# Performance work log

Measured on AMD Instinct MI355X. Metric: run time of the kernel, lower is better.

The kernel has to match this reference:

```python
import jax, jax.numpy as jnp
import numpy as np

B, L = 4, 2048
D_MODEL, D_STATE, D_CONV, EXPAND = 1024, 16, 4, 2
D_INNER = EXPAND * D_MODEL
DT_RANK = D_MODEL // 16  # mamba-ssm default dt_rank = ceil(d_model/16)


def _mamba(x, in_w, conv_w, conv_b, xproj_w, dt_w, dt_b, A_log, D, out_w):
    # x: [B, L, d_model]; faithful port of mamba_ssm.Mamba forward (slow path math)
    di, ds = A_log.shape
    dt_rank = dt_w.shape[1]
    dc = conv_w.shape[1]
    xz = x @ in_w.T                          # [B, L, 2*di]
    xi, z = jnp.split(xz, 2, axis=-1)
    # causal depthwise conv over time
    xc = jnp.swapaxes(xi, 1, 2)              # [B, di, L]
    xc = jax.lax.conv_general_dilated(
        xc, conv_w[:, None, :], (1,), [(dc - 1, 0)],
        feature_group_count=di, dimension_numbers=('NCH', 'OIH', 'NCH'))
    xc = xc + conv_b[None, :, None]
    xi = jax.nn.silu(jnp.swapaxes(xc, 1, 2))  # [B, L, di]
    proj = xi @ xproj_w.T                    # [B, L, dt_rank + 2*ds]
    dt, Bm, Cm = jnp.split(proj, [dt_rank, dt_rank + ds], axis=-1)
    delta = jax.nn.softplus(dt @ dt_w.T + dt_b)  # [B, L, di]
    A = -jnp.exp(A_log)                      # [di, ds]

    def step(h, t):
        d_t, B_t, C_t, x_t = t               # [B,di],[B,ds],[B,ds],[B,di]
        h = jnp.exp(d_t[:, :, None] * A) * h + (d_t * x_t)[:, :, None] * B_t[:, None, :]
        return h, jnp.einsum('bds,bs->bd', h, C_t)

    xs = (jnp.swapaxes(delta, 0, 1), jnp.swapaxes(Bm, 0, 1),
          jnp.swapaxes(Cm, 0, 1), jnp.swapaxes(xi, 0, 1))
    h0 = jnp.zeros((x.shape[0], di, ds), x.dtype)
    _, ys = jax.lax.scan(step, h0, xs)       # ys: [L, B, di]
    y = jnp.swapaxes(ys, 0, 1) + xi * D
    y = y * jax.nn.silu(z)
    return y @ out_w.T


def setup_inputs() -> dict:
    ks = jax.random.split(jax.random.key(0), 24)

    def p(i, shape, scale=0.02):
        return jax.random.normal(ks[i], shape, jnp.float32) * scale

    inp = {
        'x': jax.random.normal(ks[0], (B, L, D_MODEL), jnp.float32),
        'ln_g': jnp.ones((D_MODEL,), jnp.float32),
        'ln_b': jnp.zeros((D_MODEL,), jnp.float32),
        'merge_w': p(1, (D_MODEL, 2 * D_MODEL)),
        'merge_b': jnp.zeros((D_MODEL,), jnp.float32),
    }
    for j, pre in enumerate(('fwd', 'bwd')):
        o = 2 + j * 8
        inp[pre + '_in_w'] = p(o, (2 * D_INNER, D_MODEL))
        inp[pre + '_conv_w'] = p(o + 1, (D_INNER, D_CONV), 0.3)
        inp[pre + '_conv_b'] = jnp.zeros((D_INNER,), jnp.float32)
        inp[pre + '_xproj_w'] = p(o + 2, (DT_RANK + 2 * D_STATE, D_INNER))
        inp[pre + '_dt_w'] = p(o + 3, (D_INNER, DT_RANK), 0.1)
        inp[pre + '_dt_b'] = -4.0 + p(o + 4, (D_INNER,), 0.5)
        inp[pre + '_A_log'] = jnp.broadcast_to(
            jnp.log(jnp.arange(1, D_STATE + 1, dtype=jnp.float32)), (D_INNER, D_STATE)) + 0.0
        inp[pre + '_D'] = jnp.ones((D_INNER,), jnp.float32)
        inp[pre + '_out_w'] = p(o + 5, (D_MODEL, D_INNER))
    return inp


def reference(x, ln_g, ln_b, merge_w, merge_b,
              fwd_in_w, fwd_conv_w, fwd_conv_b, fwd_xproj_w, fwd_dt_w, fwd_dt_b,
              fwd_A_log, fwd_D, fwd_out_w,
              bwd_in_w, bwd_conv_w, bwd_conv_b, bwd_xproj_w, bwd_dt_w, bwd_dt_b,
              bwd_A_log, bwd_D, bwd_out_w):
    mu = jnp.mean(x, axis=-1, keepdims=True)
    var = jnp.mean(jnp.square(x - mu), axis=-1, keepdims=True)
    xn = (x - mu) / jnp.sqrt(var + 1e-5) * ln_g + ln_b
    y_f = _mamba(xn, fwd_in_w, fwd_conv_w, fwd_conv_b, fwd_xproj_w, fwd_dt_w,
                 fwd_dt_b, fwd_A_log, fwd_D, fwd_out_w)
    y_b = jnp.flip(_mamba(jnp.flip(xn, 1), bwd_in_w, bwd_conv_w, bwd_conv_b,
                          bwd_xproj_w, bwd_dt_w, bwd_dt_b, bwd_A_log, bwd_D,
                          bwd_out_w), 1)
    y = jnp.concatenate([y_f, y_b], axis=-1) @ merge_w.T + merge_b
    return x + y
```

## Files before the change

kernel.cpp:

```cpp
#include <hip/hip_runtime.h>

typedef unsigned short u16;
typedef unsigned int u32;
typedef __attribute__((ext_vector_type(8))) short short8;
typedef __attribute__((ext_vector_type(8))) u16 ushort8v;
typedef __attribute__((ext_vector_type(4))) float float4v;
typedef __attribute__((ext_vector_type(4))) u16 ushort4v;

#define SEQ_L 2048
#define NTOK 8192
#define DMODEL 1024
#define DINNER 2048
#define NCH 32
#define CHL 64

__device__ __forceinline__ float bf2f(u16 v) { return __uint_as_float(((u32)v) << 16); }
__device__ __forceinline__ u16 f2bf(float f) {
    u32 u = __float_as_uint(f);
    return (u16)((u + 0x7FFFu + ((u >> 16) & 1u)) >> 16);
}
__device__ __forceinline__ float loadf(const void* p, size_t i, bool bf) {
    return bf ? bf2f(((const u16*)p)[i]) : ((const float*)p)[i];
}
__device__ __forceinline__ void gl2lds(const void* g, void* l) {
    __builtin_amdgcn_global_load_lds(
        (const __attribute__((address_space(1))) void*)g,
        (__attribute__((address_space(3))) void*)l, 16, 0, 0);
}

__global__ void detect_kernel(const u32* __restrict__ lng, int* __restrict__ flag) {
    if (threadIdx.x == 0) flag[0] = (lng[0] == 0x3F800000u) ? 0 : 1;
}

__global__ void cvt_kernel(const void* __restrict__ in, u16* __restrict__ out,
                           int n4, const int* __restrict__ flag) {
    int i = blockIdx.x * 256 + threadIdx.x;
    if (i >= n4) return;
    bool bf = flag[0] != 0;
    ushort4v o;
    if (bf) {
        o = ((const ushort4v*)in)[i];
    } else {
        float4v v = ((const float4v*)in)[i];
        o.x = f2bf(v.x); o.y = f2bf(v.y); o.z = f2bf(v.z); o.w = f2bf(v.w);
    }
    ((ushort4v*)out)[i] = o;
}

__global__ __launch_bounds__(256) void transpose_ow(const void* __restrict__ ow,
        u16* __restrict__ ot, const int* __restrict__ flag) {
    bool bf = flag[0] != 0;
    __shared__ u16 tile[32][33];
    int k0 = blockIdx.x * 32;
    int j0 = blockIdx.y * 32;
    int tx = threadIdx.x & 31;
    int ty = threadIdx.x >> 5;
    #pragma unroll
    for (int r = 0; r < 4; ++r) {
        int j = ty + r * 8;
        tile[j][tx] = f2bf(loadf(ow, (size_t)(j0 + j) * 2048 + k0 + tx, bf));
    }
    __syncthreads();
    #pragma unroll
    for (int r = 0; r < 4; ++r) {
        int k = ty + r * 8;
        ot[(size_t)(k0 + k) * 1024 + j0 + tx] = tile[tx][k];
    }
}

__global__ __launch_bounds__(256) void ln_kernel(const void* __restrict__ xin,
        const void* __restrict__ g, const void* __restrict__ be,
        u16* __restrict__ xn, const int* __restrict__ flag) {
    bool bf = flag[0] != 0;
    int tok = blockIdx.x;
    int tid = threadIdx.x;
    float v[4];
    if (bf) {
        ushort4v u = ((const ushort4v*)xin)[(size_t)tok * 256 + tid];
        v[0] = bf2f(u.x); v[1] = bf2f(u.y); v[2] = bf2f(u.z); v[3] = bf2f(u.w);
    } else {
        float4v f = ((const float4v*)xin)[(size_t)tok * 256 + tid];
        v[0] = f.x; v[1] = f.y; v[2] = f.z; v[3] = f.w;
    }
    float s = v[0] + v[1] + v[2] + v[3];
    float s2 = v[0]*v[0] + v[1]*v[1] + v[2]*v[2] + v[3]*v[3];
    for (int o = 1; o < 64; o <<= 1) { s += __shfl_xor(s, o); s2 += __shfl_xor(s2, o); }
    __shared__ float red[8];
    int w = tid >> 6;
    if ((tid & 63) == 0) { red[w] = s; red[4 + w] = s2; }
    __syncthreads();
    s = red[0] + red[1] + red[2] + red[3];
    s2 = red[4] + red[5] + red[6] + red[7];
    float mu = s * (1.f / 1024.f);
    float var = s2 * (1.f / 1024.f) - mu * mu;
    float rstd = rsqrtf(var + 1e-5f);
    int base = tid * 4;
    ushort4v o;
    o.x = f2bf((v[0] - mu) * rstd * loadf(g, base + 0, bf) + loadf(be, base + 0, bf));
    o.y = f2bf((v[1] - mu) * rstd * loadf(g, base + 1, bf) + loadf(be, base + 1, bf));
    o.z = f2bf((v[2] - mu) * rstd * loadf(g, base + 2, bf) + loadf(be, base + 2, bf));
    o.w = f2bf((v[3] - mu) * rstd * loadf(g, base + 3, bf) + loadf(be, base + 3, bf));
    ((ushort4v*)xn)[(size_t)tok * 256 + tid] = o;
}

__global__ __launch_bounds__(256) void build_wf(
    const void* __restrict__ dtw, const void* __restrict__ xpw,
    u16* __restrict__ wf, const int* __restrict__ flag)
{
    bool bf = flag[0] != 0;
    int n = blockIdx.x;
    int k0 = threadIdx.x * 8;
    ushort8v o;
    if (n >= DINNER) {
        int r = (n - DINNER) + 64;
        if (bf) {
            o = *(const ushort8v*)((const u16*)xpw + (size_t)r * 2048 + k0);
        } else {
            const float* p = (const float*)xpw + (size_t)r * 2048 + k0;
            #pragma unroll
            for (int j = 0; j < 8; ++j) o[j] = f2bf(p[j]);
        }
    } else {
        float acc[8];
        #pragma unroll
        for (int j = 0; j < 8; ++j) acc[j] = 0.f;
        for (int r = 0; r < 64; ++r) {
            float dw = loadf(dtw, (size_t)n * 64 + r, bf);
            if (bf) {
                ushort8v v = *(const ushort8v*)((const u16*)xpw + (size_t)r * 2048 + k0);
                #pragma unroll
                for (int j = 0; j < 8; ++j) acc[j] = fmaf(dw, bf2f(v[j]), acc[j]);
            } else {
                const float* p = (const float*)xpw + (size_t)r * 2048 + k0;
                #pragma unroll
                for (int j = 0; j < 8; ++j) acc[j] = fmaf(dw, p[j], acc[j]);
            }
        }
        #pragma unroll
        for (int j = 0; j < 8; ++j) o[j] = f2bf(acc[j]);
    }
    *(ushort8v*)(wf + (size_t)n * 2048 + k0) = o;
}

template<int EPI, bool FLIPA>
__global__ __launch_bounds__(256) void gemm_bt(
    const u16* __restrict__ A, int lda,
    const u16* __restrict__ W, int ldw,
    void* __restrict__ Cv, int ldc,
    int M, int N, int K,
    const void* __restrict__ bias, const void* __restrict__ resid,
    const int* __restrict__ flag)
{
    __shared__ u16 As[128 * 32];
    __shared__ u16 Ws[128 * 32];
    bool bf = flag[0] != 0;
    int tid = threadIdx.x;
    int lane = tid & 63;
    int wave = tid >> 6;
    int wm = wave >> 1, wn = wave & 1;
    int m0 = blockIdx.x * 128;
    int n0 = blockIdx.y * 128;
    int l15 = lane & 15;
    int quad = lane >> 4;

    int c0 = tid, c1 = tid + 256;
    int row0 = c0 >> 2, row1 = c1 >> 2;
    int kk0 = ((c0 & 3) ^ ((row0 ^ (row0 >> 1)) & 3)) << 3;
    int kk1 = ((c1 & 3) ^ ((row1 ^ (row1 >> 1)) & 3)) << 3;
    int ar0 = m0 + row0, ar1 = m0 + row1;
    if (FLIPA) {
        int b0 = ar0 >> 11, t0 = ar0 & (SEQ_L - 1); ar0 = (b0 << 11) | (SEQ_L - 1 - t0);
        int b1 = ar1 >> 11, t1 = ar1 & (SEQ_L - 1); ar1 = (b1 << 11) | (SEQ_L - 1 - t1);
    }
    int wr0 = n0 + row0; if (wr0 > N - 1) wr0 = N - 1;
    int wr1 = n0 + row1; if (wr1 > N - 1) wr1 = N - 1;
    const u16* Ag0 = A + (size_t)ar0 * lda + kk0;
    const u16* Ag1 = A + (size_t)ar1 * lda + kk1;
    const u16* Wg0 = W + (size_t)wr0 * ldw + kk0;
    const u16* Wg1 = W + (size_t)wr1 * ldw + kk1;
    u16* lA0 = &As[c0 * 8]; u16* lA1 = &As[c1 * 8];
    u16* lW0 = &Ws[c0 * 8]; u16* lW1 = &Ws[c1 * 8];

    int aoff[4], boff[4];
    #pragma unroll
    for (int i = 0; i < 4; ++i) {
        int ra = wm * 64 + i * 16 + l15;
        aoff[i] = ra * 32 + ((quad ^ ((ra ^ (ra >> 1)) & 3)) << 3);
        int rb = wn * 64 + i * 16 + l15;
        boff[i] = rb * 32 + ((quad ^ ((rb ^ (rb >> 1)) & 3)) << 3);
    }

    float4v acc[4][4] = {};

    for (int k0 = 0; k0 < K; k0 += 32) {
        __syncthreads();
        gl2lds(Ag0 + k0, lA0);
        gl2lds(Ag1 + k0, lA1);
        gl2lds(Wg0 + k0, lW0);
        gl2lds(Wg1 + k0, lW1);
        __syncthreads();
        short8 af[4], bfr[4];
        #pragma unroll
        for (int i = 0; i < 4; ++i) af[i] = *(const short8*)&As[aoff[i]];
        #pragma unroll
        for (int j = 0; j < 4; ++j) bfr[j] = *(const short8*)&Ws[boff[j]];
        #pragma unroll
        for (int i = 0; i < 4; ++i)
            #pragma unroll
            for (int j = 0; j < 4; ++j)
                acc[i][j] = __builtin_amdgcn_mfma_f32_16x16x32_bf16(af[i], bfr[j], acc[i][j], 0, 0, 0);
    }

    #pragma unroll
    for (int i = 0; i < 4; ++i) {
        #pragma unroll
        for (int j = 0; j < 4; ++j) {
            #pragma unroll
            for (int r = 0; r < 4; ++r) {
                int row = m0 + wm * 64 + i * 16 + quad * 4 + r;
                int col = n0 + wn * 64 + j * 16 + l15;
                if (col < N) {
                    float v = acc[i][j][r];
                    if (EPI == 0) {
                        ((u16*)Cv)[(size_t)row * ldc + col] = f2bf(v);
                    } else if (EPI == 2) {
                        v += loadf(bias, col, bf) + loadf(resid, (size_t)row * DMODEL + col, bf);
                        if (bf) ((u16*)Cv)[(size_t)row * ldc + col] = f2bf(v);
                        else    ((float*)Cv)[(size_t)row * ldc + col] = v;
                    } else if (EPI == 3) {
                        if (col < DINNER) {
                            v += loadf(bias, col, bf);
                            v = fmaxf(v, 0.f) + __logf(1.f + __expf(-fabsf(v)));
                            ((u16*)Cv)[(size_t)row * 4096 + col] = f2bf(v);
                        } else {
                            ((u16*)resid)[(size_t)row * 32 + (col - DINNER)] = f2bf(v);
                        }
                    } else {
                        if (bf) {
                            u16* p = (u16*)Cv + (size_t)row * ldc + col;
                            *p = f2bf(bf2f(*p) + v);
                        } else {
                            float* p = (float*)Cv + (size_t)row * ldc + col;
                            *p = *p + v;
                        }
                    }
                }
            }
        }
    }
}

__global__ __launch_bounds__(256) void conv_kernel(const u16* __restrict__ xz,
        const void* __restrict__ cw, const void* __restrict__ cb,
        u16* __restrict__ xc, const int* __restrict__ flag)
{
    bool bf = flag[0] != 0;
    int idx = blockIdx.x * 256 + threadIdx.x;
    int d = idx & (DINNER - 1);
    int t = (idx >> 11) & (SEQ_L - 1);
    int b = idx >> 22;
    float acc = loadf(cb, d, bf);
    #pragma unroll
    for (int k = 0; k < 4; ++k) {
        int tt = t - 3 + k;
        if (tt >= 0)
            acc += loadf(cw, d * 4 + k, bf) * bf2f(xz[((size_t)(b * SEQ_L + tt) << 12) + d]);
    }
    float r = acc / (1.f + __expf(-acc));
    xc[idx] = f2bf(r);
}


__global__ __launch_bounds__(256) void scan_pass1(
    const u16* __restrict__ xz, const u16* __restrict__ xc,
    const u16* __restrict__ proj, const void* __restrict__ A_log,
    float2* __restrict__ chk, const int* __restrict__ flag)
{
    bool bf = flag[0] != 0;
    int g = blockIdx.x * 256 + threadIdx.x;
    int d = g & (DINNER - 1);
    int c = (g >> 11) & (NCH - 1);
    int b = g >> 16;
    float Ac[16];
    #pragma unroll
    for (int s = 0; s < 16; ++s) Ac[s] = -__expf(loadf(A_log, (size_t)d * 16 + s, bf));
    size_t tok0 = (size_t)b * SEQ_L + c * CHL;
    const u16* dp = xz + tok0 * 4096 + d;
    const u16* xp = xc + tok0 * DINNER + d;
    const u16* bp = proj + tok0 * 32;
    float h[16];
    #pragma unroll
    for (int s = 0; s < 16; ++s) h[s] = 0.f;
    float sd = 0.f;
    for (int t = 0; t < CHL; ++t) {
        float dl = bf2f(*dp);
        float xi = bf2f(*xp);
        ushort8v bv0 = *(const ushort8v*)bp;
        ushort8v bv1 = *(const ushort8v*)(bp + 8);
        float u = dl * xi;
        #pragma unroll
        for (int s = 0; s < 16; ++s) {
            float a = __expf(dl * Ac[s]);
            float Bs = bf2f(s < 8 ? bv0[s] : bv1[s - 8]);
            h[s] = fmaf(a, h[s], u * Bs);
        }
        sd += dl;
        dp += 4096; xp += DINNER; bp += 32;
    }
    size_t base = (size_t)c * 131072 + ((size_t)b << 15) + d;
    #pragma unroll
    for (int s = 0; s < 16; ++s)
        chk[base + (size_t)s * 2048] = make_float2(__expf(Ac[s] * sd), h[s]);
}

__global__ __launch_bounds__(256) void scan_mid(float2* __restrict__ chk) {
    int g = blockIdx.x * 256 + threadIdx.x;
    float hi = 0.f;
    #pragma unroll 4
    for (int c = 0; c < NCH; ++c) {
        float2 v = chk[(size_t)c * 131072 + g];
        chk[(size_t)c * 131072 + g].x = hi;
        hi = fmaf(v.x, hi, v.y);
    }
}

__global__ __launch_bounds__(256) void scan_pass2(
    u16* __restrict__ xz, const u16* __restrict__ xc,
    const u16* __restrict__ proj, const void* __restrict__ A_log,
    const void* __restrict__ Dp, const float2* __restrict__ chk,
    const int* __restrict__ flag)
{
    bool bf = flag[0] != 0;
    int g = blockIdx.x * 256 + threadIdx.x;
    int d = g & (DINNER - 1);
    int c = (g >> 11) & (NCH - 1);
    int b = g >> 16;
    float Ac[16];
    #pragma unroll
    for (int s = 0; s < 16; ++s) Ac[s] = -__expf(loadf(A_log, (size_t)d * 16 + s, bf));
    float Dd = loadf(Dp, d, bf);
    size_t tok0 = (size_t)b * SEQ_L + c * CHL;
    const u16* dp = xz + tok0 * 4096 + d;
    const u16* xp = xc + tok0 * DINNER + d;
    const u16* bp = proj + tok0 * 32;
    u16* zp = xz + tok0 * 4096 + DINNER + d;
    size_t base = (size_t)c * 131072 + ((size_t)b << 15) + d;
    float h[16];
    #pragma unroll
    for (int s = 0; s < 16; ++s) h[s] = chk[base + (size_t)s * 2048].x;
    for (int t = 0; t < CHL; ++t) {
        float dl = bf2f(*dp);
        float xi = bf2f(*xp);
        ushort8v bv0 = *(const ushort8v*)bp;
        ushort8v bv1 = *(const ushort8v*)(bp + 8);
        ushort8v cv0 = *(const ushort8v*)(bp + 16);
        ushort8v cv1 = *(const ushort8v*)(bp + 24);
        float u = dl * xi;
        float y0 = 0.f, y1 = 0.f;
        #pragma unroll
        for (int s = 0; s < 16; ++s) {
            float a = __expf(dl * Ac[s]);
            float Bs = bf2f(s < 8 ? bv0[s] : bv1[s - 8]);
            float Cs = bf2f(s < 8 ? cv0[s] : cv1[s - 8]);
            h[s] = fmaf(a, h[s], u * Bs);
            if (s & 1) y1 = fmaf(h[s], Cs, y1); else y0 = fmaf(h[s], Cs, y0);
        }
        float y = y0 + y1 + xi * Dd;
        float z = bf2f(*zp);
        *zp = f2bf(y * (z / (1.f + __expf(-z))));
        dp += 4096; xp += DINNER; bp += 32; zp += 4096;
    }
}

extern "C" void kernel_launch(void* const* d_in, const int* in_sizes, int n_in,
                              void* d_out, int out_size, void* d_ws, size_t ws_size,
                              hipStream_t stream) {
    (void)in_sizes; (void)n_in; (void)out_size;
    const void* x = d_in[0];
    const void* ln_g = d_in[1];
    const void* ln_be = d_in[2];
    const void* merge_w = d_in[3];
    const void* merge_b = d_in[4];
    const void* in_w[2]   = {d_in[5],  d_in[14]};
    const void* conv_w[2] = {d_in[6],  d_in[15]};
    const void* conv_b[2] = {d_in[7],  d_in[16]};
    const void* xproj_w[2]= {d_in[8],  d_in[17]};
    const void* dt_w[2]   = {d_in[9],  d_in[18]};
    const void* dt_bias[2]= {d_in[10], d_in[19]};
    const void* A_log[2]  = {d_in[11], d_in[20]};
    const void* Dp[2]     = {d_in[12], d_in[21]};
    const void* out_w[2]  = {d_in[13], d_in[22]};

    char* wsb = (char*)d_ws;
    size_t off = 0;
    auto alloc = [&](size_t bytes) -> void* {
        void* p = wsb + off; off += (bytes + 255) & ~(size_t)255; return p;
    };
    int* flag     = (int*)alloc(256);
    u16* xzb      = (u16*)alloc((size_t)NTOK * 4096 * 2);
    u16* xcb      = (u16*)alloc((size_t)NTOK * 2048 * 2);
    u16* projb    = (u16*)alloc((size_t)NTOK * 32 * 2);
    float2* chk   = (float2*)alloc((size_t)NCH * 131072 * 8);
    u16* wf       = (u16*)alloc((size_t)2080 * 2048 * 2);
    u16* wof[2]   = {(u16*)alloc((size_t)1024 * 2048 * 2),
                     (u16*)alloc((size_t)1024 * 2048 * 2)};
    u16* xn       = (u16*)alloc((size_t)NTOK * DMODEL * 2);
    u16* w_mgc    = (u16*)alloc((size_t)1024 * 2048 * 2);
    u16* outT     = (u16*)alloc((size_t)2048 * 1024 * 2);
    if (off > ws_size) return;

    u16* w_in = (u16*)chk;

    detect_kernel<<<1, 64, 0, stream>>>((const u32*)ln_g, flag);
    ln_kernel<<<dim3(NTOK), 256, 0, stream>>>(x, ln_g, ln_be, xn, flag);

    auto cvt = [&](const void* src, u16* dst, int n) {
        cvt_kernel<<<dim3(n / 1024), 256, 0, stream>>>(src, dst, n / 4, flag);
    };

    cvt(merge_w, w_mgc, 1024 * 2048);
    for (int dd = 0; dd < 2; ++dd) {
        transpose_ow<<<dim3(64, 32), 256, 0, stream>>>(out_w[dd], outT, flag);
        gemm_bt<0,false><<<dim3(8, 16), 256, 0, stream>>>(
            w_mgc + dd * 1024, 2048, outT, 1024, wof[dd], 2048, 1024, 2048, 1024,
            nullptr, nullptr, flag);
    }

    for (int dd = 0; dd < 2; ++dd) {
        cvt(in_w[dd], w_in, 4096 * 1024);
        if (dd == 0)
            gemm_bt<0,false><<<dim3(64,32), 256, 0, stream>>>(xn, 1024, w_in, 1024, xzb, 4096, NTOK, 4096, 1024, nullptr, nullptr, flag);
        else
            gemm_bt<0,true><<<dim3(64,32), 256, 0, stream>>>(xn, 1024, w_in, 1024, xzb, 4096, NTOK, 4096, 1024, nullptr, nullptr, flag);
        conv_kernel<<<dim3((NTOK * DINNER) / 256), 256, 0, stream>>>(xzb, conv_w[dd], conv_b[dd], xcb, flag);
        build_wf<<<dim3(2080), 256, 0, stream>>>(dt_w[dd], xproj_w[dd], wf, flag);
        gemm_bt<3,false><<<dim3(64,17), 256, 0, stream>>>(xcb, 2048, wf, 2048, xzb, 4096, NTOK, 2080, 2048, dt_bias[dd], projb, flag);
        scan_pass1<<<dim3(1024), 256, 0, stream>>>(xzb, xcb, projb, A_log[dd], chk, flag);
        scan_mid<<<dim3(512), 256, 0, stream>>>(chk);
        scan_pass2<<<dim3(1024), 256, 0, stream>>>(xzb, xcb, projb, A_log[dd], Dp[dd], chk, flag);
        if (dd == 0)
            gemm_bt<2,false><<<dim3(64,8), 256, 0, stream>>>(xzb + DINNER, 4096, wof[0], 2048, d_out, 1024, NTOK, 1024, 2048, merge_b, x, flag);
        else
            gemm_bt<5,true><<<dim3(64,8), 256, 0, stream>>>(xzb + DINNER, 4096, wof[1], 2048, d_out, 1024, NTOK, 1024, 2048, nullptr, nullptr, flag);
    }
}
```

Measured before the change: 1.375 ms.

## Double-buffer GEMM LDS tiles and vectorize causal conv kernel

```diff
diff --git a/kernel.cpp b/kernel.cpp
--- a/kernel.cpp
+++ b/kernel.cpp
@@ -151,8 +151,10 @@
     const void* __restrict__ bias, const void* __restrict__ resid,
     const int* __restrict__ flag)
 {
-    __shared__ u16 As[128 * 32];
-    __shared__ u16 Ws[128 * 32];
+    __shared__ u16 As0[128 * 32];
+    __shared__ u16 Ws0[128 * 32];
+    __shared__ u16 As1[128 * 32];
+    __shared__ u16 Ws1[128 * 32];
     bool bf = flag[0] != 0;
     int tid = threadIdx.x;
     int lane = tid & 63;
@@ -178,8 +180,7 @@
     const u16* Ag1 = A + (size_t)ar1 * lda + kk1;
     const u16* Wg0 = W + (size_t)wr0 * ldw + kk0;
     const u16* Wg1 = W + (size_t)wr1 * ldw + kk1;
-    u16* lA0 = &As[c0 * 8]; u16* lA1 = &As[c1 * 8];
-    u16* lW0 = &Ws[c0 * 8]; u16* lW1 = &Ws[c1 * 8];
+    int sc0 = c0 * 8, sc1 = c1 * 8;
 
     int aoff[4], boff[4];
     #pragma unroll
@@ -191,25 +192,44 @@
     }
 
     float4v acc[4][4] = {};
-
-    for (int k0 = 0; k0 < K; k0 += 32) {
-        __syncthreads();
-        gl2lds(Ag0 + k0, lA0);
-        gl2lds(Ag1 + k0, lA1);
-        gl2lds(Wg0 + k0, lW0);
-        gl2lds(Wg1 + k0, lW1);
-        __syncthreads();
-        short8 af[4], bfr[4];
-        #pragma unroll
-        for (int i = 0; i < 4; ++i) af[i] = *(const short8*)&As[aoff[i]];
-        #pragma unroll
-        for (int j = 0; j < 4; ++j) bfr[j] = *(const short8*)&Ws[boff[j]];
-        #pragma unroll
-        for (int i = 0; i < 4; ++i)
-            #pragma unroll
-            for (int j = 0; j < 4; ++j)
-                acc[i][j] = __builtin_amdgcn_mfma_f32_16x16x32_bf16(af[i], bfr[j], acc[i][j], 0, 0, 0);
-    }
+    int nt = K >> 5;
+
+#define STAGE_T(BA, BW, KO) \
+    gl2lds(Ag0 + (KO), &BA[sc0]); \
+    gl2lds(Ag1 + (KO), &BA[sc1]); \
+    gl2lds(Wg0 + (KO), &BW[sc0]); \
+    gl2lds(Wg1 + (KO), &BW[sc1]);
+
+#define COMPUTE_T(BA, BW) { \
+    short8 af[4], bfr[4]; \
+    _Pragma("unroll") \
+    for (int i = 0; i < 4; ++i) af[i] = *(const short8*)&BA[aoff[i]]; \
+    _Pragma("unroll") \
+    for (int j = 0; j < 4; ++j) bfr[j] = *(const short8*)&BW[boff[j]]; \
+    _Pragma("unroll") \
+    for (int i = 0; i < 4; ++i) { \
+        _Pragma("unroll") \
+        for (int j = 0; j < 4; ++j) \
+            acc[i][j] = __builtin_amdgcn_mfma_f32_16x16x32_bf16(af[i], bfr[j], acc[i][j], 0, 0, 0); \
+    } }
+
+#define SYNC_PIPE \
+    asm volatile("s_waitcnt vmcnt(0)" ::: "memory"); \
+    __builtin_amdgcn_s_barrier();
+
+    STAGE_T(As0, Ws0, 0)
+    SYNC_PIPE
+    for (int t = 0; t < nt; t += 2) {
+        STAGE_T(As1, Ws1, (t + 1) << 5)
+        COMPUTE_T(As0, Ws0)
+        SYNC_PIPE
+        if (t + 2 < nt) { STAGE_T(As0, Ws0, (t + 2) << 5) }
+        COMPUTE_T(As1, Ws1)
+        SYNC_PIPE
+    }
+#undef STAGE_T
+#undef COMPUTE_T
+#undef SYNC_PIPE
 
     #pragma unroll
     for (int i = 0; i < 4; ++i) {
@@ -255,19 +275,53 @@
         u16* __restrict__ xc, const int* __restrict__ flag)
 {
     bool bf = flag[0] != 0;
-    int idx = blockIdx.x * 256 + threadIdx.x;
-    int d = idx & (DINNER - 1);
-    int t = (idx >> 11) & (SEQ_L - 1);
-    int b = idx >> 22;
-    float acc = loadf(cb, d, bf);
+    int gid = blockIdx.x * 256 + threadIdx.x;
+    int d = (gid & 255) << 3;
+    int tok = gid >> 8;
+    int t = tok & (SEQ_L - 1);
+    int b = tok >> 11;
+    float cwf[32], acc[8];
+    if (bf) {
+        const u16* p = (const u16*)cw + d * 4;
+        #pragma unroll
+        for (int r = 0; r < 4; ++r) {
+            ushort8v v = *(const ushort8v*)(p + r * 8);
+            #pragma unroll
+            for (int j = 0; j < 8; ++j) cwf[r * 8 + j] = bf2f(v[j]);
+        }
+        ushort8v bv = *(const ushort8v*)((const u16*)cb + d);
+        #pragma unroll
+        for (int j = 0; j < 8; ++j) acc[j] = bf2f(bv[j]);
+    } else {
+        const float4v* p = (const float4v*)((const float*)cw + d * 4);
+        #pragma unroll
+        for (int r = 0; r < 8; ++r) {
+            float4v v = p[r];
+            cwf[r * 4 + 0] = v.x; cwf[r * 4 + 1] = v.y;
+            cwf[r * 4 + 2] = v.z; cwf[r * 4 + 3] = v.w;
+        }
+        const float4v* pb = (const float4v*)((const float*)cb + d);
+        float4v b0 = pb[0], b1 = pb[1];
+        acc[0] = b0.x; acc[1] = b0.y; acc[2] = b0.z; acc[3] = b0.w;
+        acc[4] = b1.x; acc[5] = b1.y; acc[6] = b1.z; acc[7] = b1.w;
+    }
+    const u16* xp = xz + (((size_t)(b * SEQ_L + t)) << 12) + d;
     #pragma unroll
     for (int k = 0; k < 4; ++k) {
         int tt = t - 3 + k;
-        if (tt >= 0)
-            acc += loadf(cw, d * 4 + k, bf) * bf2f(xz[((size_t)(b * SEQ_L + tt) << 12) + d]);
-    }
-    float r = acc / (1.f + __expf(-acc));
-    xc[idx] = f2bf(r);
+        if (tt >= 0) {
+            ushort8v xv = *(const ushort8v*)(xp + (long)(k - 3) * 4096);
+            #pragma unroll
+            for (int j = 0; j < 8; ++j) acc[j] = fmaf(cwf[j * 4 + k], bf2f(xv[j]), acc[j]);
+        }
+    }
+    ushort8v o;
+    #pragma unroll
+    for (int j = 0; j < 8; ++j) {
+        float r = acc[j] / (1.f + __expf(-acc[j]));
+        o[j] = f2bf(r);
+    }
+    *(ushort8v*)(xc + (size_t)tok * DINNER + d) = o;
 }
 
 
@@ -432,7 +486,7 @@
             gemm_bt<0,false><<<dim3(64,32), 256, 0, stream>>>(xn, 1024, w_in, 1024, xzb, 4096, NTOK, 4096, 1024, nullptr, nullptr, flag);
         else
             gemm_bt<0,true><<<dim3(64,32), 256, 0, stream>>>(xn, 1024, w_in, 1024, xzb, 4096, NTOK, 4096, 1024, nullptr, nullptr, flag);
-        conv_kernel<<<dim3((NTOK * DINNER) / 256), 256, 0, stream>>>(xzb, conv_w[dd], conv_b[dd], xcb, flag);
+        conv_kernel<<<dim3((NTOK * DINNER / 8) / 256), 256, 0, stream>>>(xzb, conv_w[dd], conv_b[dd], xcb, flag);
         build_wf<<<dim3(2080), 256, 0, stream>>>(dt_w[dd], xproj_w[dd], wf, flag);
         gemm_bt<3,false><<<dim3(64,17), 256, 0, stream>>>(xcb, 2048, wf, 2048, xzb, 4096, NTOK, 2080, 2048, dt_bias[dd], projb, flag);
         scan_pass1<<<dim3(1024), 256, 0, stream>>>(xzb, xcb, projb, A_log[dd], chk, flag);
```

Measured after the change: 1.290 ms. 1.07x faster.
